# Performance work log

Hardware: AMD Instinct MI355X
Metric: run time of the kernel (lower is better)

Reference implementation:

```python
import jax, jax.numpy as jnp
import numpy as np

L_MAX = 3
MP_SCALING = 0.1
E = 640000
N_ATOMS = 20000
K = 32


def setup_inputs() -> dict:
    key = jax.random.key(0)
    k1, k2, k3, k4, k5 = jax.random.split(key, 5)
    sh = jax.random.normal(k1, (E, (L_MAX + 1) ** 2), dtype=jnp.float32)
    radial_basis = jax.random.normal(k2, (E, L_MAX + 1, K), dtype=jnp.float32)
    center_embedding = jax.random.normal(k3, (N_ATOMS, K), dtype=jnp.float32)
    centers = jax.random.randint(k4, (E,), 0, N_ATOMS, dtype=jnp.int32)
    neighbors = jax.random.randint(k5, (E,), 0, N_ATOMS, dtype=jnp.int32)
    return {
        "sh": sh,
        "radial_basis": radial_basis,
        "center_embedding": center_embedding,
        "centers": centers,
        "neighbors": neighbors,
        "n_atoms": N_ATOMS,
    }


def reference(sh, radial_basis, center_embedding, centers, neighbors, n_atoms):
    # Gather neighbor embeddings once: [E, K]
    emb_n = center_embedding[neighbors]
    blocks = []
    off = 0
    for l in range(L_MAX + 1):
        m = 2 * l + 1
        sh_l = sh[:, off:off + m]            # [E, m]
        off += m
        rb_l = radial_basis[:, l, :]          # [E, K]
        # edge-wise product sh * radial * gathered embedding: [E, m, K]
        src = sh_l[:, :, None] * (rb_l * emb_n)[:, None, :]
        # scatter-add over center atoms -> per-atom density [n_atoms, m, K]
        dens_l = jax.ops.segment_sum(src, centers, num_segments=n_atoms)
        blocks.append(dens_l * MP_SCALING)
    # concatenate per-l blocks along the component axis: [n_atoms, sum(2l+1)=16, K]
    return jnp.concatenate(blocks, axis=1)
```

## Files before the change

kernel.cpp:

```cpp
#include <hip/hip_runtime.h>

#define KDIM 32


__global__ void hist_kernel(const int* __restrict__ centers, int* __restrict__ counts, int n) {
    int i = blockIdx.x * blockDim.x + threadIdx.x;
    if (i < n) atomicAdd(&counts[centers[i]], 1);
}

__global__ __launch_bounds__(1024) void scan_kernel(const int* __restrict__ counts,
                                                    int* __restrict__ offsets,
                                                    int* __restrict__ cursor, int n) {
    __shared__ int lds[1024];
    int t = threadIdx.x;
    int chunk = (n + 1023) >> 10;
    int s = t * chunk;
    int e = min(s + chunk, n);
    int sum = 0;
    for (int i = s; i < e; i++) sum += counts[i];
    lds[t] = sum;
    __syncthreads();
    for (int off = 1; off < 1024; off <<= 1) {
        int v = (t >= off) ? lds[t - off] : 0;
        __syncthreads();
        lds[t] += v;
        __syncthreads();
    }
    int run = lds[t] - sum;
    for (int i = s; i < e; i++) {
        int c = counts[i];
        offsets[i] = run;
        cursor[i] = run;
        run += c;
    }
    if (t == 1023) offsets[n] = run;
}

__global__ void scatter_kernel(const int* __restrict__ centers,
                               const int* __restrict__ neighbors,
                               int* __restrict__ cursor,
                               int2* __restrict__ recs, int n) {
    int i = blockIdx.x * blockDim.x + threadIdx.x;
    if (i < n) {
        int c = centers[i];
        int nn = neighbors[i];
        int pos = atomicAdd(&cursor[c], 1);
        recs[pos] = make_int2(i, nn);
    }
}


#define EDGE_BODY(EB, RP, SHP)                                            \
    {                                                                     \
        float t0 = RP[0 * KDIM + k] * EB;                                 \
        float t1 = RP[1 * KDIM + k] * EB;                                 \
        float t2 = RP[2 * KDIM + k] * EB;                                 \
        float t3 = RP[3 * KDIM + k] * EB;                                 \
        float4 sA = SHP[0];                                               \
        float4 sB = SHP[1];                                               \
        float c0 = hb ? t2 : t0;                                          \
        float c1 = hb ? t3 : t1;                                          \
        float c2 = hb ? t3 : t2;                                          \
        a0 += sA.x * c0;                                                  \
        a1 += sA.y * c1;                                                  \
        a2 += sA.z * c1;                                                  \
        a3 += sA.w * c1;                                                  \
        a4 += sB.x * c2;                                                  \
        a5 += sB.y * c2;                                                  \
        a6 += sB.z * c2;                                                  \
        a7 += sB.w * c2;                                                  \
    }

__global__ __launch_bounds__(256) void imp_main_kernel(
    const float* __restrict__ sh, const float* __restrict__ rb,
    const float* __restrict__ emb, const int2* __restrict__ recs,
    const int* __restrict__ offsets, float* __restrict__ out, int n_atoms) {
    int wid  = threadIdx.x >> 6;
    int aib  = wid >> 1;
    int half = wid & 1;
    int atom = blockIdx.x * 2 + aib;
    int lane = threadIdx.x & 63;
    int k = lane & 31;
    int h = lane >> 5;
    bool hb = (h != 0);

    __shared__ float red[2][8 * 64];

    float a0 = 0.f, a1 = 0.f, a2 = 0.f, a3 = 0.f;
    float a4 = 0.f, a5 = 0.f, a6 = 0.f, a7 = 0.f;

    bool valid = (atom < n_atoms);
    int i = 0, lim = 0;
    if (valid) {
        int start = offsets[atom];
        int end   = offsets[atom + 1];
        int cnt   = end - start;
        int mid   = start + ((cnt + 1) >> 1);
        i   = half ? mid : start;
        lim = half ? end : mid;
    }

    for (; i + 4 <= lim; i += 4) {
        int2 r0 = recs[i + 0];
        int2 r1 = recs[i + 1];
        int2 r2 = recs[i + 2];
        int2 r3 = recs[i + 3];
        int e0 = __builtin_amdgcn_readfirstlane(r0.x);
        int n0 = __builtin_amdgcn_readfirstlane(r0.y);
        int e1 = __builtin_amdgcn_readfirstlane(r1.x);
        int n1 = __builtin_amdgcn_readfirstlane(r1.y);
        int e2 = __builtin_amdgcn_readfirstlane(r2.x);
        int n2 = __builtin_amdgcn_readfirstlane(r2.y);
        int e3 = __builtin_amdgcn_readfirstlane(r3.x);
        int n3 = __builtin_amdgcn_readfirstlane(r3.y);

        float eb0 = emb[(size_t)n0 * KDIM + k];
        float eb1 = emb[(size_t)n1 * KDIM + k];
        float eb2 = emb[(size_t)n2 * KDIM + k];
        float eb3 = emb[(size_t)n3 * KDIM + k];

        const float* rp0 = rb + (size_t)e0 * (4 * KDIM);
        const float* rp1 = rb + (size_t)e1 * (4 * KDIM);
        const float* rp2 = rb + (size_t)e2 * (4 * KDIM);
        const float* rp3 = rb + (size_t)e3 * (4 * KDIM);

        const float4* sp0 = (const float4*)(sh + (size_t)e0 * 16 + 8 * h);
        const float4* sp1 = (const float4*)(sh + (size_t)e1 * 16 + 8 * h);
        const float4* sp2 = (const float4*)(sh + (size_t)e2 * 16 + 8 * h);
        const float4* sp3 = (const float4*)(sh + (size_t)e3 * 16 + 8 * h);

        EDGE_BODY(eb0, rp0, sp0)
        EDGE_BODY(eb1, rp1, sp1)
        EDGE_BODY(eb2, rp2, sp2)
        EDGE_BODY(eb3, rp3, sp3)
    }
    for (; i < lim; i++) {
        int2 r0 = recs[i];
        int e0 = __builtin_amdgcn_readfirstlane(r0.x);
        int n0 = __builtin_amdgcn_readfirstlane(r0.y);
        float eb0 = emb[(size_t)n0 * KDIM + k];
        const float* rp0 = rb + (size_t)e0 * (4 * KDIM);
        const float4* sp0 = (const float4*)(sh + (size_t)e0 * 16 + 8 * h);
        EDGE_BODY(eb0, rp0, sp0)
    }

    if (half) {
        float* rp = &red[aib][0];
        rp[0 * 64 + lane] = a0;
        rp[1 * 64 + lane] = a1;
        rp[2 * 64 + lane] = a2;
        rp[3 * 64 + lane] = a3;
        rp[4 * 64 + lane] = a4;
        rp[5 * 64 + lane] = a5;
        rp[6 * 64 + lane] = a6;
        rp[7 * 64 + lane] = a7;
    }
    __syncthreads();
    if (!half && valid) {
        const float* rp = &red[aib][0];
        a0 += rp[0 * 64 + lane];
        a1 += rp[1 * 64 + lane];
        a2 += rp[2 * 64 + lane];
        a3 += rp[3 * 64 + lane];
        a4 += rp[4 * 64 + lane];
        a5 += rp[5 * 64 + lane];
        a6 += rp[6 * 64 + lane];
        a7 += rp[7 * 64 + lane];

        const float SCALE = 0.1f;
        float* op = out + (size_t)atom * (16 * KDIM) + (size_t)(8 * h) * KDIM + k;
        op[0 * KDIM] = a0 * SCALE;
        op[1 * KDIM] = a1 * SCALE;
        op[2 * KDIM] = a2 * SCALE;
        op[3 * KDIM] = a3 * SCALE;
        op[4 * KDIM] = a4 * SCALE;
        op[5 * KDIM] = a5 * SCALE;
        op[6 * KDIM] = a6 * SCALE;
        op[7 * KDIM] = a7 * SCALE;
    }
}

extern "C" void kernel_launch(void* const* d_in, const int* in_sizes, int n_in,
                              void* d_out, int out_size, void* d_ws, size_t ws_size,
                              hipStream_t stream) {
    const float* sh        = (const float*)d_in[0];
    const float* rb        = (const float*)d_in[1];
    const float* emb       = (const float*)d_in[2];
    const int*   centers   = (const int*)d_in[3];
    const int*   neighbors = (const int*)d_in[4];

    int E = in_sizes[3];
    int N = in_sizes[2] / KDIM;

    float* out = (float*)d_out;

    int2* recs    = (int2*)d_ws;
    int*  counts  = (int*)(recs + E);
    int*  offsets = counts + N;
    int*  cursor  = offsets + N + 1;

    hipMemsetAsync(counts, 0, (size_t)N * sizeof(int), stream);

    hist_kernel<<<(E + 255) / 256, 256, 0, stream>>>(centers, counts, E);
    scan_kernel<<<1, 1024, 0, stream>>>(counts, offsets, cursor, N);
    scatter_kernel<<<(E + 255) / 256, 256, 0, stream>>>(centers, neighbors, cursor, recs, E);

    int blocks = (N + 1) / 2;
    imp_main_kernel<<<blocks, 256, 0, stream>>>(sh, rb, emb, recs, offsets, out, N);
}
```

Before: 618.8 us.

## Fuse CSR build (memset, histogram, scan, scatter) into one cooperative kernel

Replaces the memset plus three separate kernels that build the center-sorted edge list with a single cooperative kernel of 256 blocks, using grid-wide syncs between the zeroing, histogram, scan and scatter phases. The single-block serial scan becomes a two-level parallel scan across blocks. This is meant to cut launch gaps and the slow one-block scan, at the cost of grid.sync overhead and lower parallelism for the histogram and scatter phases.

After: 728.6 us. 17.7% more time.

```diff
diff --git a/kernel.cpp b/kernel.cpp
--- a/kernel.cpp
+++ b/kernel.cpp
@@ -1,48 +1,77 @@
 #include <hip/hip_runtime.h>
+#include <hip/hip_cooperative_groups.h>
+
+namespace cg = cooperative_groups;
 
 #define KDIM 32
-
-
-__global__ void hist_kernel(const int* __restrict__ centers, int* __restrict__ counts, int n) {
-    int i = blockIdx.x * blockDim.x + threadIdx.x;
-    if (i < n) atomicAdd(&counts[centers[i]], 1);
-}
-
-__global__ __launch_bounds__(1024) void scan_kernel(const int* __restrict__ counts,
-                                                    int* __restrict__ offsets,
-                                                    int* __restrict__ cursor, int n) {
-    __shared__ int lds[1024];
-    int t = threadIdx.x;
-    int chunk = (n + 1023) >> 10;
-    int s = t * chunk;
-    int e = min(s + chunk, n);
+#define CSR_BLOCKS 256
+
+__global__ __launch_bounds__(256) void csr_build_coop(
+    const int* __restrict__ centers, const int* __restrict__ neighbors,
+    int* __restrict__ counts, int* __restrict__ offsets, int* __restrict__ cursor,
+    int* __restrict__ blockSums, int2* __restrict__ recs, int E, int N) {
+    cg::grid_group grid = cg::this_grid();
+    int nb  = gridDim.x;
+    int bid = blockIdx.x;
+    int t   = threadIdx.x;
+    int gtid = bid * 256 + t;
+    int gsz  = nb * 256;
+
+    __shared__ int lds[256];
+
+    for (int i = gtid; i < N; i += gsz) counts[i] = 0;
+    grid.sync();
+
+    for (int i = gtid; i < E; i += gsz) atomicAdd(&counts[centers[i]], 1);
+    grid.sync();
+
+    int chunk = (N + nb - 1) / nb;
+    int s0 = bid * chunk;
+    int e0 = min(s0 + chunk, N);
+    int per = (chunk + 255) >> 8;
+    int ts = s0 + t * per;
+    int te = min(ts + per, e0);
     int sum = 0;
-    for (int i = s; i < e; i++) sum += counts[i];
+    for (int i = ts; i < te; i++) sum += counts[i];
     lds[t] = sum;
     __syncthreads();
-    for (int off = 1; off < 1024; off <<= 1) {
+    for (int off = 1; off < 256; off <<= 1) {
         int v = (t >= off) ? lds[t - off] : 0;
         __syncthreads();
         lds[t] += v;
         __syncthreads();
     }
-    int run = lds[t] - sum;
-    for (int i = s; i < e; i++) {
+    int texcl = lds[t] - sum;
+    if (t == 255) blockSums[bid] = lds[255];
+    grid.sync();
+
+    if (bid == 0) {
+        int v = (t < nb) ? blockSums[t] : 0;
+        __syncthreads();
+        lds[t] = v;
+        __syncthreads();
+        for (int off = 1; off < 256; off <<= 1) {
+            int w = (t >= off) ? lds[t - off] : 0;
+            __syncthreads();
+            lds[t] += w;
+            __syncthreads();
+        }
+        if (t < nb) blockSums[t] = lds[t] - v;
+        if (t == nb - 1) offsets[N] = lds[nb - 1];
+    }
+    grid.sync();
+
+    int run = blockSums[bid] + texcl;
+    for (int i = ts; i < te; i++) {
         int c = counts[i];
         offsets[i] = run;
-        cursor[i] = run;
+        cursor[i]  = run;
         run += c;
     }
-    if (t == 1023) offsets[n] = run;
-}
-
-__global__ void scatter_kernel(const int* __restrict__ centers,
-                               const int* __restrict__ neighbors,
-                               int* __restrict__ cursor,
-                               int2* __restrict__ recs, int n) {
-    int i = blockIdx.x * blockDim.x + threadIdx.x;
-    if (i < n) {
-        int c = centers[i];
+    grid.sync();
+
+    for (int i = gtid; i < E; i += gsz) {
+        int c  = centers[i];
         int nn = neighbors[i];
         int pos = atomicAdd(&cursor[c], 1);
         recs[pos] = make_int2(i, nn);
@@ -194,16 +223,17 @@
 
     float* out = (float*)d_out;
 
-    int2* recs    = (int2*)d_ws;
-    int*  counts  = (int*)(recs + E);
-    int*  offsets = counts + N;
-    int*  cursor  = offsets + N + 1;
-
-    hipMemsetAsync(counts, 0, (size_t)N * sizeof(int), stream);
-
-    hist_kernel<<<(E + 255) / 256, 256, 0, stream>>>(centers, counts, E);
-    scan_kernel<<<1, 1024, 0, stream>>>(counts, offsets, cursor, N);
-    scatter_kernel<<<(E + 255) / 256, 256, 0, stream>>>(centers, neighbors, cursor, recs, E);
+    int2* recs      = (int2*)d_ws;
+    int*  counts    = (int*)(recs + E);
+    int*  offsets   = counts + N;
+    int*  cursor    = offsets + N + 1;
+    int*  blockSums = cursor + N;
+
+    void* args[] = {(void*)&centers, (void*)&neighbors, (void*)&counts,
+                    (void*)&offsets, (void*)&cursor, (void*)&blockSums,
+                    (void*)&recs, (void*)&E, (void*)&N};
+    hipLaunchCooperativeKernel((const void*)csr_build_coop, dim3(CSR_BLOCKS),
+                               dim3(256), args, 0, stream);
 
     int blocks = (N + 1) / 2;
     imp_main_kernel<<<blocks, 256, 0, stream>>>(sh, rb, emb, recs, offsets, out, N);
```
